# Optimization experiments

Hardware: AMD Instinct MI355X
Metric: run time of the kernel (lower is better)

The kernel has to match this reference:

```python
import jax, jax.numpy as jnp
import numpy as np

N, T, C, G, E = 50000, 2, 768, 16, 800000
H = C // 4          # 192
OUT = 3
EPS = 1e-5


def _lin_init(k, fan_in, fan_out):
    s = 1.0 / np.sqrt(fan_in)
    kw, kb = jax.random.split(k)
    W = jax.random.uniform(kw, (fan_in, fan_out), minval=-s, maxval=s, dtype=jnp.float32)
    b = jax.random.uniform(kb, (fan_out,), minval=-s, maxval=s, dtype=jnp.float32)
    return W, b


def setup_inputs() -> dict:
    key = jax.random.key(0)
    ks = jax.random.split(key, 8)
    x = jax.random.normal(ks[0], (N, T, C), dtype=jnp.float32)
    batch = jnp.sort(jax.random.randint(ks[1], (N,), 0, G))
    edge_index = jax.random.randint(ks[2], (2, E), 0, N)
    W0, b0 = _lin_init(ks[3], C, H)
    W1, b1 = _lin_init(ks[4], H, H)
    Wh1, bh1 = _lin_init(ks[5], H, H)
    Wh2, bh2 = _lin_init(ks[6], H, OUT)
    ones = jnp.ones((H,), jnp.float32)
    zeros = jnp.zeros((H,), jnp.float32)
    return {
        "x": x, "batch": batch, "edge_index": edge_index,
        "W0": W0, "b0": b0, "gn0_w": ones, "gn0_b": zeros, "gn0_a": ones,
        "W1": W1, "b1": b1, "gn1_w": ones, "gn1_b": zeros, "gn1_a": ones,
        "Wh1": Wh1, "bh1": bh1, "Wh2": Wh2, "bh2": bh2,
    }


def _gelu(v):
    return jax.nn.gelu(v, approximate=False)  # torch nn.GELU default = exact erf


def _gcn_conv(h, W, b, src, dst, dinv):
    # PyG GCNConv: x' = D^-1/2 (A+I) D^-1/2 (x W) + b, self-loops added implicitly
    h = jnp.einsum('ntc,cd->ntd', h, W)                       # [N,T,Cout]
    norm = (dinv[src] * dinv[dst])[:, None, None]             # [E,1,1]
    agg = jax.ops.segment_sum(h[src] * norm, dst, num_segments=N)
    agg = agg + h * (dinv * dinv)[:, None, None]              # self-loop term
    return agg + b


def _graph_norm(h, batch, cnt, w, b, alpha):
    # PyG GraphNorm: per-graph mean/var with learnable mean scale
    mean = jax.ops.segment_sum(h, batch, num_segments=G) / cnt   # [G,T,C]
    out = h - alpha * mean[batch]
    var = jax.ops.segment_sum(out * out, batch, num_segments=G) / cnt
    std = jnp.sqrt(var + EPS)
    return w * out / std[batch] + b


def reference(x, batch, edge_index,
              W0, b0, gn0_w, gn0_b, gn0_a,
              W1, b1, gn1_w, gn1_b, gn1_a,
              Wh1, bh1, Wh2, bh2):
    src, dst = edge_index[0], edge_index[1]
    deg = jax.ops.segment_sum(jnp.ones((E,), jnp.float32), dst, num_segments=N) + 1.0
    dinv = jax.lax.rsqrt(deg)
    cnt = jax.ops.segment_sum(jnp.ones((N,), jnp.float32), batch, num_segments=G)[:, None, None]

    # layer 0: 768 -> 192 (no residual, shape mismatch)
    h = _gcn_conv(x, W0, b0, src, dst, dinv)
    h = _gelu(_graph_norm(h, batch, cnt, gn0_w, gn0_b, gn0_a))
    # layer 1: 192 -> 192 with residual
    h_in = h
    h = _gcn_conv(h, W1, b1, src, dst, dinv)
    h = _gelu(_graph_norm(h, batch, cnt, gn1_w, gn1_b, gn1_a))
    h = h + h_in
    # MLP head
    h = _gelu(jnp.einsum('ntc,cd->ntd', h, Wh1) + bh1)
    out = jnp.einsum('ntc,cd->ntd', h, Wh2) + bh2            # [N,T,3]
    return out
```

## Files before the change

kernel.cpp:

```cpp
#include <hip/hip_runtime.h>
#include <math.h>

#define NN   50000
#define TT   2
#define CC   768
#define GG   16
#define EE   800000
#define HH   192
#define OUTD 3
#define MR   (NN*TT)
#define FD   (TT*HH)
#define EPS_GN 1e-5f
#define GN_CHUNK 32
#define AGG_CH 128

typedef __attribute__((ext_vector_type(8))) short bf16x8;
typedef __attribute__((ext_vector_type(4))) float f32x4;

__device__ __forceinline__ float gelu_exact(float x){
    return 0.5f * x * (1.0f + erff(x * 0.70710678118654752440f));
}

__device__ __forceinline__ short f2b(float f){
    unsigned u = __float_as_uint(f);
    unsigned r = (u + 0x7FFFu + ((u>>16)&1u)) >> 16;
    return (short)r;
}
__device__ __forceinline__ float b2f(unsigned short u){
    return __uint_as_float(((unsigned)u)<<16);
}

__global__ __launch_bounds__(256) void k_deg(const int* __restrict__ dst, float* __restrict__ deg){
    int e = blockIdx.x*256 + threadIdx.x;
    if(e < EE) atomicAdd(&deg[dst[e]], 1.0f);
}

__global__ __launch_bounds__(64) void k_cnt2(const int* __restrict__ batch, float* __restrict__ cnt){
    int g = threadIdx.x;
    if(g >= GG) return;
    int lo0=0, hi=NN;
    while(lo0<hi){ int mid=(lo0+hi)>>1; if(batch[mid] < g) lo0=mid+1; else hi=mid; }
    int lo1=lo0; hi=NN;
    while(lo1<hi){ int mid=(lo1+hi)>>1; if(batch[mid] < g+1) lo1=mid+1; else hi=mid; }
    cnt[g] = (float)(lo1 - lo0);
}

__global__ __launch_bounds__(256) void k_wconv(const float* __restrict__ W0, const float* __restrict__ W1,
                                               const float* __restrict__ Wh1,
                                               short* __restrict__ Wt0, short* __restrict__ Wt1,
                                               short* __restrict__ Wth1){
    int i = blockIdx.x*256 + threadIdx.x;
    if(i < CC*HH){
        int k = i / HH, n = i % HH;
        Wt0[(size_t)n*CC + k] = f2b(W0[i]);
    }
    if(i < HH*HH){
        int k = i / HH, n = i % HH;
        Wt1 [(size_t)n*HH + k] = f2b(W1[i]);
        Wth1[(size_t)n*HH + k] = f2b(Wh1[i]);
    }
}

__global__ __launch_bounds__(256) void k_scan1(const float* __restrict__ deg, int* __restrict__ partial,
                                               float* __restrict__ dinv){
    __shared__ int s[256];
    int t = threadIdx.x;
    int i = blockIdx.x*256 + t;
    float dv = (i < NN) ? deg[i] : 0.f;
    if(i < NN) dinv[i] = rsqrtf(dv + 1.0f);
    int v = (int)dv;
    s[t] = v; __syncthreads();
    for(int off=128; off>0; off>>=1){ if(t < off) s[t] += s[t+off]; __syncthreads(); }
    if(t == 0) partial[blockIdx.x] = s[0];
}

__global__ __launch_bounds__(256) void k_scan2(int* __restrict__ partial){
    __shared__ int s[256];
    int t = threadIdx.x;
    int v = partial[t];
    s[t] = v; __syncthreads();
    for(int off=1; off<256; off<<=1){
        int x = (t >= off) ? s[t-off] : 0;
        __syncthreads();
        s[t] += x;
        __syncthreads();
    }
    partial[t] = s[t] - v;
}

__global__ __launch_bounds__(256) void k_scan3(const float* __restrict__ deg, const int* __restrict__ partial,
                                               int* __restrict__ csr_off){
    __shared__ int s[256];
    int t = threadIdx.x;
    int i = blockIdx.x*256 + t;
    int v = (i < NN) ? (int)deg[i] : 0;
    s[t] = v; __syncthreads();
    for(int off=1; off<256; off<<=1){
        int x = (t >= off) ? s[t-off] : 0;
        __syncthreads();
        s[t] += x;
        __syncthreads();
    }
    if(i < NN) csr_off[i] = partial[blockIdx.x] + s[t] - v;
}

__global__ __launch_bounds__(256) void k_fill(const int* __restrict__ src, const int* __restrict__ dst,
                                              const int* __restrict__ csr_off, int* __restrict__ fillcnt,
                                              int* __restrict__ csr_src){
    int e = blockIdx.x*256 + threadIdx.x;
    if(e < EE){
        int d = dst[e];
        int pos = csr_off[d] + atomicAdd(&fillcnt[d], 1);
        csr_src[pos] = src[e];
    }
}

__device__ __forceinline__ void gn8r(float4 u0, float4 u1,
                                     const float* __restrict__ sm, const float* __restrict__ sq,
                                     int sb, int hb_,
                                     const float* __restrict__ wg, const float* __restrict__ bg,
                                     const float* __restrict__ ag, float ic, float v[8]){
    float4 m0 = *(const float4*)(sm+sb),   m1 = *(const float4*)(sm+sb+4);
    float4 q0 = *(const float4*)(sq+sb),   q1 = *(const float4*)(sq+sb+4);
    float4 w0 = *(const float4*)(wg+hb_),  w1 = *(const float4*)(wg+hb_+4);
    float4 b0 = *(const float4*)(bg+hb_),  b1 = *(const float4*)(bg+hb_+4);
    float4 a0 = *(const float4*)(ag+hb_),  a1 = *(const float4*)(ag+hb_+4);
    float uu[8]={u0.x,u0.y,u0.z,u0.w,u1.x,u1.y,u1.z,u1.w};
    float mm[8]={m0.x,m0.y,m0.z,m0.w,m1.x,m1.y,m1.z,m1.w};
    float qq[8]={q0.x,q0.y,q0.z,q0.w,q1.x,q1.y,q1.z,q1.w};
    float ww[8]={w0.x,w0.y,w0.z,w0.w,w1.x,w1.y,w1.z,w1.w};
    float bb[8]={b0.x,b0.y,b0.z,b0.w,b1.x,b1.y,b1.z,b1.w};
    float aa[8]={a0.x,a0.y,a0.z,a0.w,a1.x,a1.y,a1.z,a1.w};
    #pragma unroll
    for(int j=0;j<8;j++){
        float mean = mm[j]*ic, ex2 = qq[j]*ic, al = aa[j];
        float var = ex2 - (2.0f*al - al*al)*mean*mean;
        float t = ww[j]*(uu[j] - al*mean)*rsqrtf(var + EPS_GN) + bb[j];
        v[j] = gelu_exact(t);
    }
}

template<int MODE, int NORM, bool BIAS>
__global__ __launch_bounds__(256) void k_gemm_mfma(
        const float* __restrict__ A1, const float* __restrict__ A0,
        const short* __restrict__ Bt,
        const float* __restrict__ bias, void* __restrict__ Cv,
        const float* __restrict__ W2, const float* __restrict__ b2,
        const int* __restrict__ batch, const float* __restrict__ cnt,
        const float* __restrict__ sm1, const float* __restrict__ sq1,
        const float* __restrict__ wg1, const float* __restrict__ bg1, const float* __restrict__ ag1,
        const float* __restrict__ sm0, const float* __restrict__ sq0,
        const float* __restrict__ wg0, const float* __restrict__ bg0, const float* __restrict__ ag0,
        int Mrows, int Kdim){
    __shared__ short As[64][40];
    __shared__ short Bs[192][40];
    int tid = threadIdx.x;
    int bm = blockIdx.x*64;
    int wv = tid>>6, lane = tid&63;
    int lm = lane&15, lq = lane>>4;

    f32x4 acc[12];
    #pragma unroll
    for(int i=0;i<12;i++) acc[i] = (f32x4){0.f,0.f,0.f,0.f};

    int ar = tid>>2, akg = (tid&3)<<3;
    int row = bm + ar;
    bool aok = row < Mrows;
    const float* Ap1 = A1 + (size_t)row*Kdim + akg;
    const float* Ap0 = (NORM==2) ? (A0 + (size_t)row*Kdim + akg) : nullptr;
    int g = 0, tT = 0; float ic = 0.f;
    if(NORM >= 1 && aok){
        int nn = row>>1; tT = row&1;
        g = batch[nn];
        ic = 1.0f / cnt[g];
    }

    float4 ra0 = make_float4(0,0,0,0), ra1 = ra0, rb0 = ra0, rb1 = ra0;
    bf16x8 bv[3];
    if(aok){
        ra0 = *(const float4*)(Ap1); ra1 = *(const float4*)(Ap1 + 4);
        if(NORM==2){ rb0 = *(const float4*)(Ap0); rb1 = *(const float4*)(Ap0 + 4); }
    }
    #pragma unroll
    for(int i=0;i<3;i++){
        int idx = tid + i*256;
        int n = idx>>2, kg = (idx&3)<<3;
        bv[i] = *(const bf16x8*)(Bt + (size_t)n*Kdim + kg);
    }

    for(int k0 = 0; k0 < Kdim; k0 += 32){
        bf16x8 ap = {};
        if(aok){
            if(NORM == 0){
                ap[0]=f2b(ra0.x); ap[1]=f2b(ra0.y); ap[2]=f2b(ra0.z); ap[3]=f2b(ra0.w);
                ap[4]=f2b(ra1.x); ap[5]=f2b(ra1.y); ap[6]=f2b(ra1.z); ap[7]=f2b(ra1.w);
            } else {
                int hb_ = akg + k0;
                int sb  = g*FD + tT*HH + hb_;
                float v[8];
                gn8r(ra0, ra1, sm1, sq1, sb, hb_, wg1, bg1, ag1, ic, v);
                if(NORM == 2){
                    float v0[8];
                    gn8r(rb0, rb1, sm0, sq0, sb, hb_, wg0, bg0, ag0, ic, v0);
                    #pragma unroll
                    for(int j=0;j<8;j++) v[j] += v0[j];
                }
                #pragma unroll
                for(int j=0;j<8;j++) ap[j] = f2b(v[j]);
            }
        }
        bf16x8 bw0 = bv[0], bw1 = bv[1], bw2 = bv[2];
        __syncthreads();
        *(bf16x8*)&As[ar][akg] = ap;
        {
            int idx0 = tid, idx1 = tid+256, idx2 = tid+512;
            *(bf16x8*)&Bs[idx0>>2][(idx0&3)<<3] = bw0;
            *(bf16x8*)&Bs[idx1>>2][(idx1&3)<<3] = bw1;
            *(bf16x8*)&Bs[idx2>>2][(idx2&3)<<3] = bw2;
        }
        __syncthreads();
        int k1 = k0 + 32;
        if(k1 < Kdim){
            if(aok){
                ra0 = *(const float4*)(Ap1 + k1); ra1 = *(const float4*)(Ap1 + k1 + 4);
                if(NORM==2){ rb0 = *(const float4*)(Ap0 + k1); rb1 = *(const float4*)(Ap0 + k1 + 4); }
            }
            #pragma unroll
            for(int i=0;i<3;i++){
                int idx = tid + i*256;
                int n = idx>>2, kg = (idx&3)<<3;
                bv[i] = *(const bf16x8*)(Bt + (size_t)n*Kdim + k1 + kg);
            }
        }
        bf16x8 af = *(const bf16x8*)&As[wv*16 + lm][lq*8];
        #pragma unroll
        for(int ct=0; ct<12; ct++){
            bf16x8 bfr = *(const bf16x8*)&Bs[ct*16 + lm][lq*8];
            acc[ct] = __builtin_amdgcn_mfma_f32_16x16x32_bf16(af, bfr, acc[ct], 0, 0, 0);
        }
    }

    if(MODE == 1){
        short* C = (short*)Cv;
        #pragma unroll
        for(int ct=0; ct<12; ct++){
            int col = ct*16 + lm;
            float bs = BIAS ? bias[col] : 0.f;
            #pragma unroll
            for(int r=0; r<4; r++){
                int orow = bm + wv*16 + lq*4 + r;
                if(orow < Mrows) C[(size_t)orow*HH + col] = f2b(acc[ct][r] + bs);
            }
        }
    } else {
        float hs[4][3] = {};
        #pragma unroll
        for(int ct=0; ct<12; ct++){
            int col = ct*16 + lm;
            float bs = bias[col];
            float w20 = W2[col*3+0], w21 = W2[col*3+1], w22 = W2[col*3+2];
            #pragma unroll
            for(int r=0; r<4; r++){
                float gl = gelu_exact(acc[ct][r] + bs);
                hs[r][0] += gl*w20; hs[r][1] += gl*w21; hs[r][2] += gl*w22;
            }
        }
        #pragma unroll
        for(int off=1; off<16; off<<=1){
            #pragma unroll
            for(int r=0;r<4;r++){
                hs[r][0] += __shfl_xor(hs[r][0], off);
                hs[r][1] += __shfl_xor(hs[r][1], off);
                hs[r][2] += __shfl_xor(hs[r][2], off);
            }
        }
        if(lm == 0){
            float* O = (float*)Cv;
            #pragma unroll
            for(int r=0;r<4;r++){
                int orow = bm + wv*16 + lq*4 + r;
                if(orow < Mrows){
                    O[(size_t)orow*3+0] = hs[r][0] + b2[0];
                    O[(size_t)orow*3+1] = hs[r][1] + b2[1];
                    O[(size_t)orow*3+2] = hs[r][2] + b2[2];
                }
            }
        }
    }
}

__global__ __launch_bounds__(192) void k_agg(const ushort* __restrict__ hw, const int* __restrict__ csr_src,
                                             const int* __restrict__ csr_off, const float* __restrict__ deg,
                                             const float* __restrict__ dinv, const float* __restrict__ bias,
                                             float* __restrict__ out){
    __shared__ int   sidx[AGG_CH];
    __shared__ float swt [AGG_CH];
    int n = blockIdx.x;
    int t = threadIdx.x;
    float di = dinv[n];
    const ushort2* H2 = (const ushort2*)hw;
    ushort2 sv = H2[(size_t)n*192 + t];
    float self = di*di;
    float ax = b2f(sv.x)*self, ay = b2f(sv.y)*self;
    int beg = csr_off[n];
    int end = beg + (int)deg[n];
    for(int base = beg; base < end; base += AGG_CH){
        int m = min(AGG_CH, end - base);
        __syncthreads();
        for(int j = t; j < m; j += 192){
            int s = csr_src[base + j];
            sidx[j] = s;
            swt[j] = dinv[s]*di;
        }
        __syncthreads();
        int j = 0;
        for(; j+8 <= m; j += 8){
            int   si[8]; float wt[8]; ushort2 vv[8];
            #pragma unroll
            for(int q=0;q<8;q++){ si[q]=sidx[j+q]; wt[q]=swt[j+q]; }
            #pragma unroll
            for(int q=0;q<8;q++) vv[q] = H2[(size_t)si[q]*192 + t];
            #pragma unroll
            for(int q=0;q<8;q++){ ax += wt[q]*b2f(vv[q].x); ay += wt[q]*b2f(vv[q].y); }
        }
        for(; j < m; j++){
            int s = sidx[j]; float ww = swt[j];
            ushort2 v = H2[(size_t)s*192 + t];
            ax += ww*b2f(v.x); ay += ww*b2f(v.y);
        }
    }
    int f = 2*t;
    int hh = (f < HH) ? f : f - HH;
    out[(size_t)n*FD + f]   = ax + bias[hh];
    out[(size_t)n*FD + f+1] = ay + bias[hh+1];
}

__global__ __launch_bounds__(384) void k_gn_stats(const float* __restrict__ h, const int* __restrict__ batch,
                                                  float* __restrict__ ssum, float* __restrict__ ssq){
    int f = threadIdx.x;
    int n0 = blockIdx.x*GN_CHUNK;
    int n1 = min(n0 + GN_CHUNK, NN);
    int g = batch[n0];
    float a = 0.f, a2 = 0.f;
    int n = n0;
    for(; n+4 <= n1; n += 4){
        float v0 = h[(size_t)n*FD + f];
        float v1 = h[(size_t)(n+1)*FD + f];
        float v2 = h[(size_t)(n+2)*FD + f];
        float v3 = h[(size_t)(n+3)*FD + f];
        int b3 = batch[n+3];
        if(b3 == g){
            a  += v0+v1+v2+v3;
            a2 += v0*v0+v1*v1+v2*v2+v3*v3;
        } else {
            float vv[4] = {v0,v1,v2,v3};
            #pragma unroll
            for(int q=0;q<4;q++){
                int gn = batch[n+q];
                if(gn != g){
                    atomicAdd(&ssum[g*FD + f], a);
                    atomicAdd(&ssq [g*FD + f], a2);
                    a = 0.f; a2 = 0.f; g = gn;
                }
                a += vv[q]; a2 += vv[q]*vv[q];
            }
        }
    }
    for(; n < n1; n++){
        int gn = batch[n];
        if(gn != g){
            atomicAdd(&ssum[g*FD + f], a);
            atomicAdd(&ssq [g*FD + f], a2);
            a = 0.f; a2 = 0.f; g = gn;
        }
        float v = h[(size_t)n*FD + f];
        a += v; a2 += v*v;
    }
    atomicAdd(&ssum[g*FD + f], a);
    atomicAdd(&ssq [g*FD + f], a2);
}

extern "C" void kernel_launch(void* const* d_in, const int* in_sizes, int n_in,
                              void* d_out, int out_size, void* d_ws, size_t ws_size,
                              hipStream_t stream){
    const float* x     = (const float*)d_in[0];
    const int*   batch = (const int*)d_in[1];
    const int*   ei    = (const int*)d_in[2];
    const int*   src   = ei;
    const int*   dst   = ei + EE;
    const float* W0    = (const float*)d_in[3];
    const float* b0    = (const float*)d_in[4];
    const float* gn0_w = (const float*)d_in[5];
    const float* gn0_b = (const float*)d_in[6];
    const float* gn0_a = (const float*)d_in[7];
    const float* W1    = (const float*)d_in[8];
    const float* b1    = (const float*)d_in[9];
    const float* gn1_w = (const float*)d_in[10];
    const float* gn1_b = (const float*)d_in[11];
    const float* gn1_a = (const float*)d_in[12];
    const float* Wh1   = (const float*)d_in[13];
    const float* bh1   = (const float*)d_in[14];
    const float* Wh2   = (const float*)d_in[15];
    const float* bh2   = (const float*)d_in[16];
    float* out = (float*)d_out;

    char* w = (char*)d_ws;
    auto alloc = [&](size_t bytes)->void*{
        void* p = (void*)w;
        w += (bytes + 255) & ~(size_t)255;
        return p;
    };
    char* zbase = w;
    float* deg     = (float*)alloc((size_t)NN*4);
    int*   fillcnt = (int*)  alloc((size_t)NN*4);
    int*   partial = (int*)  alloc(256*4);
    float* s0m     = (float*)alloc((size_t)GG*FD*4);
    float* s0q     = (float*)alloc((size_t)GG*FD*4);
    float* s1m     = (float*)alloc((size_t)GG*FD*4);
    float* s1q     = (float*)alloc((size_t)GG*FD*4);
    size_t zbytes = (size_t)(w - zbase);
    float* cnt     = (float*)alloc((size_t)GG*4);
    float* dinv    = (float*)alloc((size_t)NN*4);
    int*   csr_off = (int*)  alloc((size_t)NN*4);
    int*   csr_src = (int*)  alloc((size_t)EE*4);
    short* Wt0     = (short*)alloc((size_t)HH*CC*2);
    short* Wt1     = (short*)alloc((size_t)HH*HH*2);
    short* Wth1    = (short*)alloc((size_t)HH*HH*2);
    short* hb0     = (short*)alloc((size_t)MR*HH*2);
    short* hb1     = (short*)alloc((size_t)MR*HH*2);
    float* agg0    = (float*)alloc((size_t)MR*HH*4);
    float* agg1    = (float*)alloc((size_t)MR*HH*4);

    hipMemsetAsync(zbase, 0, zbytes, stream);

    k_deg  <<<(EE+255)/256, 256, 0, stream>>>(dst, deg);
    k_cnt2 <<<1, 64, 0, stream>>>(batch, cnt);
    k_wconv<<<(CC*HH+255)/256, 256, 0, stream>>>(W0, W1, Wh1, Wt0, Wt1, Wth1);

    int nscan = (NN+255)/256;
    k_scan1<<<nscan, 256, 0, stream>>>(deg, partial, dinv);
    k_scan2<<<1,     256, 0, stream>>>(partial);
    k_scan3<<<nscan, 256, 0, stream>>>(deg, partial, csr_off);
    k_fill <<<(EE+255)/256, 256, 0, stream>>>(src, dst, csr_off, fillcnt, csr_src);

    int gemm_grid = (MR+63)/64;
    int ngn = (NN + GN_CHUNK - 1)/GN_CHUNK;

    k_gemm_mfma<1,0,false><<<gemm_grid, 256, 0, stream>>>(
        x, nullptr, Wt0, nullptr, hb0, nullptr, nullptr,
        nullptr, nullptr,
        nullptr, nullptr, nullptr, nullptr, nullptr,
        nullptr, nullptr, nullptr, nullptr, nullptr, MR, CC);
    k_agg<<<NN, 192, 0, stream>>>((const ushort*)hb0, csr_src, csr_off, deg, dinv, b0, agg0);
    k_gn_stats<<<ngn, 384, 0, stream>>>(agg0, batch, s0m, s0q);

    k_gemm_mfma<1,1,false><<<gemm_grid, 256, 0, stream>>>(
        agg0, nullptr, Wt1, nullptr, hb1, nullptr, nullptr,
        batch, cnt,
        s0m, s0q, gn0_w, gn0_b, gn0_a,
        nullptr, nullptr, nullptr, nullptr, nullptr, MR, HH);
    k_agg<<<NN, 192, 0, stream>>>((const ushort*)hb1, csr_src, csr_off, deg, dinv, b1, agg1);
    k_gn_stats<<<ngn, 384, 0, stream>>>(agg1, batch, s1m, s1q);

    k_gemm_mfma<2,2,true><<<gemm_grid, 256, 0, stream>>>(
        agg1, agg0, Wth1, bh1, out, Wh2, bh2,
        batch, cnt,
        s1m, s1q, gn1_w, gn1_b, gn1_a,
        s0m, s0q, gn0_w, gn0_b, gn0_a, MR, HH);
}
```

Measured before the change: 985.9 us.

## Fuse GraphNorm statistics into aggregation via replicated atomics and drop stats kernel

The aggregation kernel now accumulates per-graph sums and sums of squares right after producing each node's output. It scatters them with float atomics into 8 replicated buffers keyed by node index, and a small reduce kernel then collapses the replicas. This removes the separate stats pass that re-read the full aggregated activations. The separate group-count kernel is also folded into the single-block scan kernel to save a launch. The trade-off is four global atomics per thread per node, and because nodes are sorted by graph, heavy contention on a few addresses is possible.

```diff
diff --git a/kernel.cpp b/kernel.cpp
--- a/kernel.cpp
+++ b/kernel.cpp
@@ -11,8 +11,8 @@
 #define MR   (NN*TT)
 #define FD   (TT*HH)
 #define EPS_GN 1e-5f
-#define GN_CHUNK 32
 #define AGG_CH 128
+#define NREP 8
 
 typedef __attribute__((ext_vector_type(8))) short bf16x8;
 typedef __attribute__((ext_vector_type(4))) float f32x4;
@@ -33,16 +33,6 @@
 __global__ __launch_bounds__(256) void k_deg(const int* __restrict__ dst, float* __restrict__ deg){
     int e = blockIdx.x*256 + threadIdx.x;
     if(e < EE) atomicAdd(&deg[dst[e]], 1.0f);
-}
-
-__global__ __launch_bounds__(64) void k_cnt2(const int* __restrict__ batch, float* __restrict__ cnt){
-    int g = threadIdx.x;
-    if(g >= GG) return;
-    int lo0=0, hi=NN;
-    while(lo0<hi){ int mid=(lo0+hi)>>1; if(batch[mid] < g) lo0=mid+1; else hi=mid; }
-    int lo1=lo0; hi=NN;
-    while(lo1<hi){ int mid=(lo1+hi)>>1; if(batch[mid] < g+1) lo1=mid+1; else hi=mid; }
-    cnt[g] = (float)(lo1 - lo0);
 }
 
 __global__ __launch_bounds__(256) void k_wconv(const float* __restrict__ W0, const float* __restrict__ W1,
@@ -74,9 +64,18 @@
     if(t == 0) partial[blockIdx.x] = s[0];
 }
 
-__global__ __launch_bounds__(256) void k_scan2(int* __restrict__ partial){
+__global__ __launch_bounds__(256) void k_scan2(int* __restrict__ partial, const int* __restrict__ batch,
+                                               float* __restrict__ cnt){
     __shared__ int s[256];
     int t = threadIdx.x;
+    if(t < GG){
+        int g = t;
+        int lo0=0, hi=NN;
+        while(lo0<hi){ int mid=(lo0+hi)>>1; if(batch[mid] < g) lo0=mid+1; else hi=mid; }
+        int lo1=lo0; hi=NN;
+        while(lo1<hi){ int mid=(lo1+hi)>>1; if(batch[mid] < g+1) lo1=mid+1; else hi=mid; }
+        cnt[g] = (float)(lo1 - lo0);
+    }
     int v = partial[t];
     s[t] = v; __syncthreads();
     for(int off=1; off<256; off<<=1){
@@ -292,7 +291,9 @@
 __global__ __launch_bounds__(192) void k_agg(const ushort* __restrict__ hw, const int* __restrict__ csr_src,
                                              const int* __restrict__ csr_off, const float* __restrict__ deg,
                                              const float* __restrict__ dinv, const float* __restrict__ bias,
-                                             float* __restrict__ out){
+                                             const int* __restrict__ batch,
+                                             float* __restrict__ out,
+                                             float* __restrict__ ssum8, float* __restrict__ ssq8){
     __shared__ int   sidx[AGG_CH];
     __shared__ float swt [AGG_CH];
     int n = blockIdx.x;
@@ -331,53 +332,30 @@
     }
     int f = 2*t;
     int hh = (f < HH) ? f : f - HH;
-    out[(size_t)n*FD + f]   = ax + bias[hh];
-    out[(size_t)n*FD + f+1] = ay + bias[hh+1];
-}
-
-__global__ __launch_bounds__(384) void k_gn_stats(const float* __restrict__ h, const int* __restrict__ batch,
-                                                  float* __restrict__ ssum, float* __restrict__ ssq){
-    int f = threadIdx.x;
-    int n0 = blockIdx.x*GN_CHUNK;
-    int n1 = min(n0 + GN_CHUNK, NN);
-    int g = batch[n0];
-    float a = 0.f, a2 = 0.f;
-    int n = n0;
-    for(; n+4 <= n1; n += 4){
-        float v0 = h[(size_t)n*FD + f];
-        float v1 = h[(size_t)(n+1)*FD + f];
-        float v2 = h[(size_t)(n+2)*FD + f];
-        float v3 = h[(size_t)(n+3)*FD + f];
-        int b3 = batch[n+3];
-        if(b3 == g){
-            a  += v0+v1+v2+v3;
-            a2 += v0*v0+v1*v1+v2*v2+v3*v3;
-        } else {
-            float vv[4] = {v0,v1,v2,v3};
-            #pragma unroll
-            for(int q=0;q<4;q++){
-                int gn = batch[n+q];
-                if(gn != g){
-                    atomicAdd(&ssum[g*FD + f], a);
-                    atomicAdd(&ssq [g*FD + f], a2);
-                    a = 0.f; a2 = 0.f; g = gn;
-                }
-                a += vv[q]; a2 += vv[q]*vv[q];
-            }
-        }
-    }
-    for(; n < n1; n++){
-        int gn = batch[n];
-        if(gn != g){
-            atomicAdd(&ssum[g*FD + f], a);
-            atomicAdd(&ssq [g*FD + f], a2);
-            a = 0.f; a2 = 0.f; g = gn;
-        }
-        float v = h[(size_t)n*FD + f];
-        a += v; a2 += v*v;
-    }
-    atomicAdd(&ssum[g*FD + f], a);
-    atomicAdd(&ssq [g*FD + f], a2);
+    float vx = ax + bias[hh];
+    float vy = ay + bias[hh+1];
+    out[(size_t)n*FD + f]   = vx;
+    out[(size_t)n*FD + f+1] = vy;
+    int g = batch[n];
+    size_t sbase = ((size_t)(n & (NREP-1))*GG + g)*FD + f;
+    atomicAdd(&ssum8[sbase],   vx);
+    atomicAdd(&ssum8[sbase+1], vy);
+    atomicAdd(&ssq8 [sbase],   vx*vx);
+    atomicAdd(&ssq8 [sbase+1], vy*vy);
+}
+
+__global__ __launch_bounds__(256) void k_gn_reduce(const float* __restrict__ sm8, const float* __restrict__ sq8,
+                                                   float* __restrict__ fm, float* __restrict__ fq){
+    int i = blockIdx.x*256 + threadIdx.x;
+    if(i < GG*FD){
+        float a = 0.f, b = 0.f;
+        #pragma unroll
+        for(int r=0;r<NREP;r++){
+            a += sm8[(size_t)r*GG*FD + i];
+            b += sq8[(size_t)r*GG*FD + i];
+        }
+        fm[i] = a; fq[i] = b;
+    }
 }
 
 extern "C" void kernel_launch(void* const* d_in, const int* in_sizes, int n_in,
@@ -414,11 +392,15 @@
     float* deg     = (float*)alloc((size_t)NN*4);
     int*   fillcnt = (int*)  alloc((size_t)NN*4);
     int*   partial = (int*)  alloc(256*4);
-    float* s0m     = (float*)alloc((size_t)GG*FD*4);
-    float* s0q     = (float*)alloc((size_t)GG*FD*4);
-    float* s1m     = (float*)alloc((size_t)GG*FD*4);
-    float* s1q     = (float*)alloc((size_t)GG*FD*4);
+    float* s0m8    = (float*)alloc((size_t)NREP*GG*FD*4);
+    float* s0q8    = (float*)alloc((size_t)NREP*GG*FD*4);
+    float* s1m8    = (float*)alloc((size_t)NREP*GG*FD*4);
+    float* s1q8    = (float*)alloc((size_t)NREP*GG*FD*4);
     size_t zbytes = (size_t)(w - zbase);
+    float* f0m     = (float*)alloc((size_t)GG*FD*4);
+    float* f0q     = (float*)alloc((size_t)GG*FD*4);
+    float* f1m     = (float*)alloc((size_t)GG*FD*4);
+    float* f1q     = (float*)alloc((size_t)GG*FD*4);
     float* cnt     = (float*)alloc((size_t)GG*4);
     float* dinv    = (float*)alloc((size_t)NN*4);
     int*   csr_off = (int*)  alloc((size_t)NN*4);
@@ -434,37 +416,38 @@
     hipMemsetAsync(zbase, 0, zbytes, stream);
 
     k_deg  <<<(EE+255)/256, 256, 0, stream>>>(dst, deg);
-    k_cnt2 <<<1, 64, 0, stream>>>(batch, cnt);
     k_wconv<<<(CC*HH+255)/256, 256, 0, stream>>>(W0, W1, Wh1, Wt0, Wt1, Wth1);
 
     int nscan = (NN+255)/256;
     k_scan1<<<nscan, 256, 0, stream>>>(deg, partial, dinv);
-    k_scan2<<<1,     256, 0, stream>>>(partial);
+    k_scan2<<<1,     256, 0, stream>>>(partial, batch, cnt);
     k_scan3<<<nscan, 256, 0, stream>>>(deg, partial, csr_off);
     k_fill <<<(EE+255)/256, 256, 0, stream>>>(src, dst, csr_off, fillcnt, csr_src);
 
     int gemm_grid = (MR+63)/64;
-    int ngn = (NN + GN_CHUNK - 1)/GN_CHUNK;
+    int nred = (GG*FD + 255)/256;
 
     k_gemm_mfma<1,0,false><<<gemm_grid, 256, 0, stream>>>(
         x, nullptr, Wt0, nullptr, hb0, nullptr, nullptr,
         nullptr, nullptr,
         nullptr, nullptr, nullptr, nullptr, nullptr,
         nullptr, nullptr, nullptr, nullptr, nullptr, MR, CC);
-    k_agg<<<NN, 192, 0, stream>>>((const ushort*)hb0, csr_src, csr_off, deg, dinv, b0, agg0);
-    k_gn_stats<<<ngn, 384, 0, stream>>>(agg0, batch, s0m, s0q);
+    k_agg<<<NN, 192, 0, stream>>>((const ushort*)hb0, csr_src, csr_off, deg, dinv, b0, batch,
+                                  agg0, s0m8, s0q8);
+    k_gn_reduce<<<nred, 256, 0, stream>>>(s0m8, s0q8, f0m, f0q);
 
     k_gemm_mfma<1,1,false><<<gemm_grid, 256, 0, stream>>>(
         agg0, nullptr, Wt1, nullptr, hb1, nullptr, nullptr,
         batch, cnt,
-        s0m, s0q, gn0_w, gn0_b, gn0_a,
+        f0m, f0q, gn0_w, gn0_b, gn0_a,
         nullptr, nullptr, nullptr, nullptr, nullptr, MR, HH);
-    k_agg<<<NN, 192, 0, stream>>>((const ushort*)hb1, csr_src, csr_off, deg, dinv, b1, agg1);
-    k_gn_stats<<<ngn, 384, 0, stream>>>(agg1, batch, s1m, s1q);
+    k_agg<<<NN, 192, 0, stream>>>((const ushort*)hb1, csr_src, csr_off, deg, dinv, b1, batch,
+                                  agg1, s1m8, s1q8);
+    k_gn_reduce<<<nred, 256, 0, stream>>>(s1m8, s1q8, f1m, f1q);
 
     k_gemm_mfma<2,2,true><<<gemm_grid, 256, 0, stream>>>(
         agg1, agg0, Wth1, bh1, out, Wh2, bh2,
         batch, cnt,
-        s1m, s1q, gn1_w, gn1_b, gn1_a,
-        s0m, s0q, gn0_w, gn0_b, gn0_a, MR, HH);
-}
+        f1m, f1q, gn1_w, gn1_b, gn1_a,
+        f0m, f0q, gn0_w, gn0_b, gn0_a, MR, HH);
+}
```

Result: slower. 2.172 ms (+120.3%).

## Aggregate one node per wavefront with shuffle-broadcast edges instead of per-block LDS

Applied to the files above, without the earlier changes.

The GCN aggregation kernel now assigns one node per 64-lane wavefront, four nodes per block, instead of one node per 192-thread block. Edge indices and weights are loaded one per lane and broadcast with shuffles, which removes the shared-memory staging and block barriers. Each lane accumulates six features through three 4-byte loads per neighbor. Separately, the per-graph count kernel is merged into the single-block scan kernel to save a launch. The 12-byte per-lane stride gives less regular coalescing than before, and each lane holds more registers.

```diff
diff --git a/kernel.cpp b/kernel.cpp
--- a/kernel.cpp
+++ b/kernel.cpp
@@ -12,7 +12,6 @@
 #define FD   (TT*HH)
 #define EPS_GN 1e-5f
 #define GN_CHUNK 32
-#define AGG_CH 128
 
 typedef __attribute__((ext_vector_type(8))) short bf16x8;
 typedef __attribute__((ext_vector_type(4))) float f32x4;
@@ -33,16 +32,6 @@
 __global__ __launch_bounds__(256) void k_deg(const int* __restrict__ dst, float* __restrict__ deg){
     int e = blockIdx.x*256 + threadIdx.x;
     if(e < EE) atomicAdd(&deg[dst[e]], 1.0f);
-}
-
-__global__ __launch_bounds__(64) void k_cnt2(const int* __restrict__ batch, float* __restrict__ cnt){
-    int g = threadIdx.x;
-    if(g >= GG) return;
-    int lo0=0, hi=NN;
-    while(lo0<hi){ int mid=(lo0+hi)>>1; if(batch[mid] < g) lo0=mid+1; else hi=mid; }
-    int lo1=lo0; hi=NN;
-    while(lo1<hi){ int mid=(lo1+hi)>>1; if(batch[mid] < g+1) lo1=mid+1; else hi=mid; }
-    cnt[g] = (float)(lo1 - lo0);
 }
 
 __global__ __launch_bounds__(256) void k_wconv(const float* __restrict__ W0, const float* __restrict__ W1,
@@ -74,9 +63,18 @@
     if(t == 0) partial[blockIdx.x] = s[0];
 }
 
-__global__ __launch_bounds__(256) void k_scan2(int* __restrict__ partial){
+__global__ __launch_bounds__(256) void k_scan2(int* __restrict__ partial, const int* __restrict__ batch,
+                                               float* __restrict__ cnt){
     __shared__ int s[256];
     int t = threadIdx.x;
+    if(t < GG){
+        int g = t;
+        int lo0=0, hi=NN;
+        while(lo0<hi){ int mid=(lo0+hi)>>1; if(batch[mid] < g) lo0=mid+1; else hi=mid; }
+        int lo1=lo0; hi=NN;
+        while(lo1<hi){ int mid=(lo1+hi)>>1; if(batch[mid] < g+1) lo1=mid+1; else hi=mid; }
+        cnt[g] = (float)(lo1 - lo0);
+    }
     int v = partial[t];
     s[t] = v; __syncthreads();
     for(int off=1; off<256; off<<=1){
@@ -289,50 +287,62 @@
     }
 }
 
-__global__ __launch_bounds__(192) void k_agg(const ushort* __restrict__ hw, const int* __restrict__ csr_src,
+__global__ __launch_bounds__(256) void k_agg(const ushort* __restrict__ hw, const int* __restrict__ csr_src,
                                              const int* __restrict__ csr_off, const float* __restrict__ deg,
                                              const float* __restrict__ dinv, const float* __restrict__ bias,
                                              float* __restrict__ out){
-    __shared__ int   sidx[AGG_CH];
-    __shared__ float swt [AGG_CH];
-    int n = blockIdx.x;
-    int t = threadIdx.x;
+    int lane = threadIdx.x & 63;
+    int n = blockIdx.x*4 + (threadIdx.x>>6);
+    if(n >= NN) return;
     float di = dinv[n];
     const ushort2* H2 = (const ushort2*)hw;
-    ushort2 sv = H2[(size_t)n*192 + t];
+    size_t rb = (size_t)n*192 + lane*3;
+    ushort2 s0v = H2[rb], s1v = H2[rb+1], s2v = H2[rb+2];
     float self = di*di;
-    float ax = b2f(sv.x)*self, ay = b2f(sv.y)*self;
+    float a0 = b2f(s0v.x)*self, a1 = b2f(s0v.y)*self;
+    float a2 = b2f(s1v.x)*self, a3 = b2f(s1v.y)*self;
+    float a4 = b2f(s2v.x)*self, a5 = b2f(s2v.y)*self;
     int beg = csr_off[n];
     int end = beg + (int)deg[n];
-    for(int base = beg; base < end; base += AGG_CH){
-        int m = min(AGG_CH, end - base);
-        __syncthreads();
-        for(int j = t; j < m; j += 192){
-            int s = csr_src[base + j];
-            sidx[j] = s;
-            swt[j] = dinv[s]*di;
-        }
-        __syncthreads();
+    for(int base = beg; base < end; base += 64){
+        int m = min(64, end - base);
+        int e = 0; float we = 0.f;
+        if(lane < m){ e = csr_src[base + lane]; we = dinv[e]*di; }
         int j = 0;
-        for(; j+8 <= m; j += 8){
-            int   si[8]; float wt[8]; ushort2 vv[8];
-            #pragma unroll
-            for(int q=0;q<8;q++){ si[q]=sidx[j+q]; wt[q]=swt[j+q]; }
-            #pragma unroll
-            for(int q=0;q<8;q++) vv[q] = H2[(size_t)si[q]*192 + t];
-            #pragma unroll
-            for(int q=0;q<8;q++){ ax += wt[q]*b2f(vv[q].x); ay += wt[q]*b2f(vv[q].y); }
+        for(; j+4 <= m; j += 4){
+            int   sA=__shfl(e,j),  sB=__shfl(e,j+1),  sC=__shfl(e,j+2),  sD=__shfl(e,j+3);
+            float wA=__shfl(we,j), wB=__shfl(we,j+1), wC=__shfl(we,j+2), wD=__shfl(we,j+3);
+            size_t bA=(size_t)sA*192+lane*3, bB=(size_t)sB*192+lane*3;
+            size_t bC=(size_t)sC*192+lane*3, bD=(size_t)sD*192+lane*3;
+            ushort2 vA0=H2[bA], vA1=H2[bA+1], vA2=H2[bA+2];
+            ushort2 vB0=H2[bB], vB1=H2[bB+1], vB2=H2[bB+2];
+            ushort2 vC0=H2[bC], vC1=H2[bC+1], vC2=H2[bC+2];
+            ushort2 vD0=H2[bD], vD1=H2[bD+1], vD2=H2[bD+2];
+            a0 += wA*b2f(vA0.x)+wB*b2f(vB0.x)+wC*b2f(vC0.x)+wD*b2f(vD0.x);
+            a1 += wA*b2f(vA0.y)+wB*b2f(vB0.y)+wC*b2f(vC0.y)+wD*b2f(vD0.y);
+            a2 += wA*b2f(vA1.x)+wB*b2f(vB1.x)+wC*b2f(vC1.x)+wD*b2f(vD1.x);
+            a3 += wA*b2f(vA1.y)+wB*b2f(vB1.y)+wC*b2f(vC1.y)+wD*b2f(vD1.y);
+            a4 += wA*b2f(vA2.x)+wB*b2f(vB2.x)+wC*b2f(vC2.x)+wD*b2f(vD2.x);
+            a5 += wA*b2f(vA2.y)+wB*b2f(vB2.y)+wC*b2f(vC2.y)+wD*b2f(vD2.y);
         }
         for(; j < m; j++){
-            int s = sidx[j]; float ww = swt[j];
-            ushort2 v = H2[(size_t)s*192 + t];
-            ax += ww*b2f(v.x); ay += ww*b2f(v.y);
-        }
-    }
-    int f = 2*t;
-    int hh = (f < HH) ? f : f - HH;
-    out[(size_t)n*FD + f]   = ax + bias[hh];
-    out[(size_t)n*FD + f+1] = ay + bias[hh+1];
+            int s = __shfl(e, j); float ww = __shfl(we, j);
+            size_t sb = (size_t)s*192 + lane*3;
+            ushort2 v0=H2[sb], v1=H2[sb+1], v2=H2[sb+2];
+            a0 += ww*b2f(v0.x); a1 += ww*b2f(v0.y);
+            a2 += ww*b2f(v1.x); a3 += ww*b2f(v1.y);
+            a4 += ww*b2f(v2.x); a5 += ww*b2f(v2.y);
+        }
+    }
+    int f0 = lane*6;
+    float r[6] = {a0,a1,a2,a3,a4,a5};
+    float* O = out + (size_t)n*FD + f0;
+    #pragma unroll
+    for(int i=0;i<6;i++){
+        int f = f0 + i;
+        int hh = (f < HH) ? f : f - HH;
+        O[i] = r[i] + bias[hh];
+    }
 }
 
 __global__ __launch_bounds__(384) void k_gn_stats(const float* __restrict__ h, const int* __restrict__ batch,
@@ -434,16 +444,16 @@
     hipMemsetAsync(zbase, 0, zbytes, stream);
 
     k_deg  <<<(EE+255)/256, 256, 0, stream>>>(dst, deg);
-    k_cnt2 <<<1, 64, 0, stream>>>(batch, cnt);
     k_wconv<<<(CC*HH+255)/256, 256, 0, stream>>>(W0, W1, Wh1, Wt0, Wt1, Wth1);
 
     int nscan = (NN+255)/256;
     k_scan1<<<nscan, 256, 0, stream>>>(deg, partial, dinv);
-    k_scan2<<<1,     256, 0, stream>>>(partial);
+    k_scan2<<<1,     256, 0, stream>>>(partial, batch, cnt);
     k_scan3<<<nscan, 256, 0, stream>>>(deg, partial, csr_off);
     k_fill <<<(EE+255)/256, 256, 0, stream>>>(src, dst, csr_off, fillcnt, csr_src);
 
     int gemm_grid = (MR+63)/64;
+    int agg_grid  = (NN+3)/4;
     int ngn = (NN + GN_CHUNK - 1)/GN_CHUNK;
 
     k_gemm_mfma<1,0,false><<<gemm_grid, 256, 0, stream>>>(
@@ -451,7 +461,7 @@
         nullptr, nullptr,
         nullptr, nullptr, nullptr, nullptr, nullptr,
         nullptr, nullptr, nullptr, nullptr, nullptr, MR, CC);
-    k_agg<<<NN, 192, 0, stream>>>((const ushort*)hb0, csr_src, csr_off, deg, dinv, b0, agg0);
+    k_agg<<<agg_grid, 256, 0, stream>>>((const ushort*)hb0, csr_src, csr_off, deg, dinv, b0, agg0);
     k_gn_stats<<<ngn, 384, 0, stream>>>(agg0, batch, s0m, s0q);
 
     k_gemm_mfma<1,1,false><<<gemm_grid, 256, 0, stream>>>(
@@ -459,7 +469,7 @@
         batch, cnt,
         s0m, s0q, gn0_w, gn0_b, gn0_a,
         nullptr, nullptr, nullptr, nullptr, nullptr, MR, HH);
-    k_agg<<<NN, 192, 0, stream>>>((const ushort*)hb1, csr_src, csr_off, deg, dinv, b1, agg1);
+    k_agg<<<agg_grid, 256, 0, stream>>>((const ushort*)hb1, csr_src, csr_off, deg, dinv, b1, agg1);
     k_gn_stats<<<ngn, 384, 0, stream>>>(agg1, batch, s1m, s1q);
 
     k_gemm_mfma<2,2,true><<<gemm_grid, 256, 0, stream>>>(
```

After: 973.3 us. No clear change (-1.3%).
